# Kernel optimization log

Hardware: AMD Instinct MI355X
Metric: run time of the kernel (lower is better)

Reference implementation:

```python
import jax, jax.numpy as jnp
import numpy as np

B, NS, NT = 4, 512, 512
D_IN, C1, R, C2 = 128, 64, 32, 32
E = 32768
STEPS = 10


def setup_inputs() -> dict:
    key = jax.random.key(0)
    ks = jax.random.split(key, 12)
    inp = {}
    inp['x_s'] = jax.random.normal(ks[0], (B * NS, D_IN), jnp.float32)
    inp['edge_index_s'] = jax.random.randint(ks[1], (2, E), 0, B * NS, jnp.int32)
    inp['edge_attr_s'] = jax.random.uniform(ks[2], (E,), jnp.float32)
    inp['batch_s'] = (jnp.arange(B * NS, dtype=jnp.int32) // NS)
    inp['x_t'] = jax.random.normal(ks[3], (B * NT, D_IN), jnp.float32)
    inp['edge_index_t'] = jax.random.randint(ks[4], (2, E), 0, B * NT, jnp.int32)
    inp['edge_attr_t'] = jax.random.uniform(ks[5], (E,), jnp.float32)
    inp['batch_t'] = (jnp.arange(B * NT, dtype=jnp.int32) // NT)
    inp['W1'] = jax.random.normal(ks[6], (D_IN, C1), jnp.float32) / np.float32(np.sqrt(D_IN))
    inp['W2'] = jax.random.normal(ks[7], (R, C2), jnp.float32) / np.float32(np.sqrt(R))
    inp['mw1'] = jax.random.normal(ks[8], (C2, C2), jnp.float32) / np.float32(np.sqrt(C2))
    inp['mb1'] = jnp.zeros((C2,), jnp.float32)
    inp['mw2'] = jax.random.normal(ks[9], (C2, 1), jnp.float32) / np.float32(np.sqrt(C2))
    inp['mb2'] = jnp.zeros((1,), jnp.float32)
    inp['r'] = jax.random.normal(ks[10], (STEPS, B, NS, R), jnp.float32)
    return inp


def psi(x, src, dst, ea, W, n):
    # simple message-passing GNN: edge-weighted neighbor aggregation + linear + ReLU
    m = jax.ops.segment_sum(x[src] * ea[:, None], dst, num_segments=n)
    return jax.nn.relu((x + m) @ W)


def reference(x_s, edge_index_s, edge_attr_s, batch_s, x_t, edge_index_t, edge_attr_t,
              batch_t, W1, W2, mw1, mb1, mw2, mb2, r):
    # Uniform graph sizes -> to_dense_batch is a reshape and all masks are True,
    # so masked_softmax reduces to plain softmax; batch_s/batch_t kept for interface fidelity.
    ss, ds = edge_index_s[0], edge_index_s[1]
    st, dt = edge_index_t[0], edge_index_t[1]
    h_s = psi(x_s, ss, ds, edge_attr_s, W1, B * NS).reshape(B, NS, C1)
    h_t = psi(x_t, st, dt, edge_attr_t, W1, B * NT).reshape(B, NT, C1)
    S_hat0 = jnp.einsum('bsc,btc->bst', h_s, h_t)  # [B, NS, NT]
    S_0 = jax.nn.softmax(S_hat0, axis=-1)

    def step(S_hat, r_i):
        S = jax.nn.softmax(S_hat, axis=-1)
        r_t = jnp.einsum('bst,bsr->btr', S, r_i)  # S^T @ r_s
        o_s = psi(r_i.reshape(B * NS, R), ss, ds, edge_attr_s, W2, B * NS).reshape(B, NS, C2)
        o_t = psi(r_t.reshape(B * NT, R), st, dt, edge_attr_t, W2, B * NT).reshape(B, NT, C2)
        Dm = o_s[:, :, None, :] - o_t[:, None, :, :]  # [B, NS, NT, C2] outer difference
        upd = (jax.nn.relu(Dm @ mw1 + mb1) @ mw2 + mb2)[..., 0]
        return S_hat + upd, None

    S_hat, _ = jax.lax.scan(step, S_hat0, r)
    S_L = jax.nn.softmax(S_hat, axis=-1)
    return (S_0, S_L)
```

## Files before the change

kernel.cpp:

```cpp
#include <hip/hip_runtime.h>


constexpr int kB = 4;
constexpr int kNS = 512;
constexpr int kNT = 512;
constexpr int kDin = 128;
constexpr int kC1 = 64;
constexpr int kR = 32;
constexpr int kC2 = 32;
constexpr int kE = 32768;
constexpr int kSteps = 10;
constexpr int kN = kB * kNS;
constexpr int kEP = kE + 16 * kN;
constexpr int kChunkStride = kR * kN;

__global__ void k_hist(const int* __restrict__ ei_s, const int* __restrict__ ei_t,
                       int* __restrict__ deg) {
  int g = blockIdx.y;
  const int* dst = (g ? ei_t : ei_s) + kE;
  int e = blockIdx.x * 256 + threadIdx.x;
  atomicAdd(&deg[g * kN + dst[e]], 1);
}

__global__ void k_scan(const int* __restrict__ deg, int* __restrict__ off,
                       int* __restrict__ cur) {
  int g = blockIdx.x;
  const int* d = deg + g * kN;
  int* o = off + g * (kN + 1);
  int* c = cur + g * kN;
  __shared__ int sums[256];
  int tid = threadIdx.x;
  int loc[8];
  int s = 0;
#pragma unroll
  for (int i = 0; i < 8; ++i) {
    loc[i] = (d[tid * 8 + i] + 15) & ~15;
    s += loc[i];
  }
  sums[tid] = s;
  __syncthreads();
  for (int st = 1; st < 256; st <<= 1) {
    int v = (tid >= st) ? sums[tid - st] : 0;
    __syncthreads();
    sums[tid] += v;
    __syncthreads();
  }
  int base = (tid > 0) ? sums[tid - 1] : 0;
#pragma unroll
  for (int i = 0; i < 8; ++i) {
    int idx = tid * 8 + i;
    o[idx] = base;
    c[idx] = base;
    base += loc[i];
  }
  if (tid == 255) o[kN] = base;
}

__global__ void k_scatter(const int* __restrict__ ei_s, const int* __restrict__ ei_t,
                          const float* __restrict__ ea_s, const float* __restrict__ ea_t,
                          int* __restrict__ cur, int* __restrict__ srcs,
                          float* __restrict__ eaw) {
  int g = blockIdx.y;
  const int* ei = g ? ei_t : ei_s;
  const float* ea = g ? ea_t : ea_s;
  int e = blockIdx.x * 256 + threadIdx.x;
  int d = ei[kE + e];
  int srcv = ei[e];
  int pos = atomicAdd(&cur[g * kN + d], 1);
  srcs[g * kEP + pos] = srcv;
  eaw[g * kEP + pos] = ea[e];
}

__device__ __forceinline__ void psi2_node(
    int n, const float* __restrict__ vin, const int* __restrict__ sr,
    const float* __restrict__ ew, const int* __restrict__ o,
    const float* __restrict__ W2, const float* __restrict__ mw1,
    const float* __restrict__ mb1, const float* __restrict__ mw2w,
    float* __restrict__ Pout, float* __restrict__ ctOut) {
  int lane = threadIdx.x & 63;
  int f = lane & 31, hh = lane >> 5;
  int beg = o[n], end = o[n + 1];
  float m = 0.f;
  for (int b0 = beg + hh * 8; b0 < end; b0 += 16) {
#pragma unroll
    for (int q = 0; q < 8; ++q)
      m += vin[(size_t)sr[b0 + q] * kR + f] * ew[b0 + q];
  }
  m += __shfl_down(m, 32, 64);
  float v = vin[(size_t)n * kR + f] + m;
  float acc = 0.f;
#pragma unroll
  for (int k = 0; k < kC2; ++k) acc += __shfl(v, k, 64) * W2[k * kC2 + f];
  float ov = fmaxf(acc, 0.f);
  float p = mb1 ? mb1[f] : 0.f;
#pragma unroll
  for (int k = 0; k < kC2; ++k) p += __shfl(ov, k, 64) * mw1[k * kC2 + f];
  if (lane < 32) Pout[(size_t)n * kC2 + f] = p;
  if (ctOut) {
    float c = p * mw2w[f];
#pragma unroll
    for (int o2 = 16; o2; o2 >>= 1) c += __shfl_xor(c, o2, 64);
    if (lane == 0) ctOut[n] = c;
  }
}

__global__ __launch_bounds__(256) void k_pre(
    const float* __restrict__ x_s, const float* __restrict__ x_t,
    const float* __restrict__ r, const int* __restrict__ srcs,
    const float* __restrict__ eaw, const int* __restrict__ off,
    const float* __restrict__ W1, const float* __restrict__ W2,
    const float* __restrict__ mw1, const float* __restrict__ mb1,
    float* __restrict__ h, float* __restrict__ PsAll) {
  int bid = blockIdx.x, tid = threadIdx.x;
  if (bid < 2048) {
    int g = bid >> 10;
    int n = (bid & 1023) * 2 + (tid >> 7);
    int f = tid & 127;
    const float* x = g ? x_t : x_s;
    const int* sr = srcs + g * kEP;
    const float* ew = eaw + g * kEP;
    const int* o = off + g * (kN + 1);
    float* ho = h + (size_t)g * kN * kC1;
    __shared__ float y[2][kDin];
    int beg = o[n], end = o[n + 1];
    float xself = x[(size_t)n * kDin + f];
    float m = 0.f;
    for (int idx = beg; idx < end; idx += 8) {
      float a0 = x[(size_t)sr[idx + 0] * kDin + f] * ew[idx + 0];
      float a1 = x[(size_t)sr[idx + 1] * kDin + f] * ew[idx + 1];
      float a2 = x[(size_t)sr[idx + 2] * kDin + f] * ew[idx + 2];
      float a3 = x[(size_t)sr[idx + 3] * kDin + f] * ew[idx + 3];
      float a4 = x[(size_t)sr[idx + 4] * kDin + f] * ew[idx + 4];
      float a5 = x[(size_t)sr[idx + 5] * kDin + f] * ew[idx + 5];
      float a6 = x[(size_t)sr[idx + 6] * kDin + f] * ew[idx + 6];
      float a7 = x[(size_t)sr[idx + 7] * kDin + f] * ew[idx + 7];
      m += ((a0 + a1) + (a2 + a3)) + ((a4 + a5) + (a6 + a7));
    }
    y[tid >> 7][f] = xself + m;
    __syncthreads();
    if (f < kC1) {
      const float* yy = y[tid >> 7];
      float acc = 0.f;
#pragma unroll 16
      for (int k = 0; k < kDin; ++k) acc += yy[k] * W1[k * kC1 + f];
      ho[(size_t)n * kC1 + f] = fmaxf(acc, 0.f);
    }
  } else {
    int nn = (bid - 2048) * 4 + (tid >> 6);
    int step = nn >> 11, node = nn & (kN - 1);
    psi2_node(node, r + (size_t)step * kN * kR, srcs, eaw, off, W2, mw1, mb1,
              nullptr, PsAll + (size_t)step * kN * kR, nullptr);
  }
}

__global__ __launch_bounds__(256) void k_shat0(const float* __restrict__ h,
                                               float* __restrict__ Shat,
                                               float* __restrict__ pstatm,
                                               float* __restrict__ pstatl) {
  int b = blockIdx.z, s0 = blockIdx.y * 64, t0 = blockIdx.x * 64;
  const float* hs = h + (size_t)(b * kNS + s0) * kC1;
  const float* ht = h + (size_t)kN * kC1 + (size_t)(b * kNT + t0) * kC1;
  __shared__ float As[64 * 68];
  __shared__ float Bs[64 * 68];
  int tid = threadIdx.x;
#pragma unroll
  for (int k2 = 0; k2 < 4; ++k2) {
    int idx = tid + k2 * 256;
    int row = idx >> 4, c4 = idx & 15;
    float4 va = *(const float4*)(hs + (size_t)row * kC1 + c4 * 4);
    *(float4*)&As[row * 68 + c4 * 4] = va;
    float4 vb = *(const float4*)(ht + (size_t)row * kC1 + c4 * 4);
    *(float4*)&Bs[row * 68 + c4 * 4] = vb;
  }
  __syncthreads();
  int ts = tid >> 4, tt = tid & 15;
  float acc[4][4] = {};
#pragma unroll
  for (int cc = 0; cc < 16; ++cc) {
    float4 a[4], bt[4];
#pragma unroll
    for (int i = 0; i < 4; ++i) a[i] = *(const float4*)&As[(ts * 4 + i) * 68 + cc * 4];
#pragma unroll
    for (int k = 0; k < 4; ++k) bt[k] = *(const float4*)&Bs[(tt + 16 * k) * 68 + cc * 4];
#pragma unroll
    for (int i = 0; i < 4; ++i)
#pragma unroll
      for (int k = 0; k < 4; ++k)
        acc[i][k] += a[i].x * bt[k].x + a[i].y * bt[k].y + a[i].z * bt[k].z + a[i].w * bt[k].w;
  }
#pragma unroll
  for (int i = 0; i < 4; ++i) {
    int s = s0 + ts * 4 + i;
    float* row = Shat + (size_t)(b * kNS + s) * kNT;
#pragma unroll
    for (int k = 0; k < 4; ++k) row[t0 + tt + 16 * k] = acc[i][k];
  }
#pragma unroll
  for (int i = 0; i < 4; ++i) {
    float mm = fmaxf(fmaxf(acc[i][0], acc[i][1]), fmaxf(acc[i][2], acc[i][3]));
#pragma unroll
    for (int o2 = 8; o2; o2 >>= 1) mm = fmaxf(mm, __shfl_xor(mm, o2, 64));
    float se = 0.f;
#pragma unroll
    for (int k = 0; k < 4; ++k) se += __expf(acc[i][k] - mm);
#pragma unroll
    for (int o2 = 8; o2; o2 >>= 1) se += __shfl_xor(se, o2, 64);
    if (tt == 0) {
      int grow = b * kNS + s0 + ts * 4 + i;
      pstatm[blockIdx.x * kN + grow] = mm;
      pstatl[blockIdx.x * kN + grow] = se;
    }
  }
}

__global__ __launch_bounds__(256) void k_rt(const float* __restrict__ Shat,
                                            const float* __restrict__ pstatm,
                                            const float* __restrict__ pstatl,
                                            const float* __restrict__ ri,
                                            float* __restrict__ part, int nc,
                                            float* __restrict__ Sout) {
  int b = blockIdx.z, cs = blockIdx.y, s0 = cs * 64, t0 = blockIdx.x * 32;
  __shared__ float Wt[64 * 32];
  __shared__ float rch[64 * 32];
  __shared__ float lm[64], ll[64];
  int tid = threadIdx.x;
  if (tid < 64) {
    int row = b * kNS + s0 + tid;
    float m = -3.4e38f;
    for (int c = 0; c < nc; ++c) m = fmaxf(m, pstatm[c * kN + row]);
    float l = 0.f;
    for (int c = 0; c < nc; ++c) l += __expf(pstatm[c * kN + row] - m) * pstatl[c * kN + row];
    lm[tid] = m;
    ll[tid] = 1.f / l;
  }
  __syncthreads();
#pragma unroll
  for (int k2 = 0; k2 < 2; ++k2) {
    int idx = tid + k2 * 256;
    int row = idx >> 3, c4 = idx & 7;
    int grow = b * kNS + s0 + row;
    float4 v = *(const float4*)(Shat + (size_t)grow * kNT + t0 + c4 * 4);
    float m = lm[row], l = ll[row];
    float4 wv;
    wv.x = __expf(v.x - m) * l;
    wv.y = __expf(v.y - m) * l;
    wv.z = __expf(v.z - m) * l;
    wv.w = __expf(v.w - m) * l;
    *(float4*)&Wt[row * 32 + c4 * 4] = wv;
    if (Sout) *(float4*)(Sout + (size_t)grow * kNT + t0 + c4 * 4) = wv;
    float4 rv = *(const float4*)(ri + (size_t)grow * kR + c4 * 4);
    *(float4*)&rch[row * 32 + c4 * 4] = rv;
  }
  __syncthreads();
  int t_l = tid & 31, jg = tid >> 5;
  float4 acc = make_float4(0.f, 0.f, 0.f, 0.f);
  for (int s = 0; s < 64; ++s) {
    float wv = Wt[s * 32 + t_l];
    float4 rv = *(const float4*)&rch[s * 32 + jg * 4];
    acc.x += wv * rv.x; acc.y += wv * rv.y; acc.z += wv * rv.z; acc.w += wv * rv.w;
  }
  int gcol = b * kNT + t0 + t_l;
  float* dst = part + (size_t)cs * kChunkStride + (size_t)jg * 4 * kN + gcol;
  dst[0] = acc.x;
  dst[(size_t)kN] = acc.y;
  dst[(size_t)2 * kN] = acc.z;
  dst[(size_t)3 * kN] = acc.w;
}

__global__ __launch_bounds__(256) void k_red(const float* __restrict__ part,
                                             float* __restrict__ rt) {
  int idx = blockIdx.x * 256 + threadIdx.x;
  int j = idx >> 11, col = idx & (kN - 1);
  float s = 0.f;
#pragma unroll
  for (int cs = 0; cs < 8; ++cs) s += part[(size_t)cs * kChunkStride + idx];
  rt[(size_t)col * kR + j] = s;
}

__global__ __launch_bounds__(256) void k_psi2t(
    const float* __restrict__ rt, const int* __restrict__ srcs,
    const float* __restrict__ eaw, const int* __restrict__ off,
    const float* __restrict__ W2, const float* __restrict__ mw1,
    const float* __restrict__ mw2, float* __restrict__ Pt,
    float* __restrict__ ct) {
  int n = blockIdx.x * 4 + (threadIdx.x >> 6);
  psi2_node(n, rt, srcs + kEP, eaw + kEP, off + (kN + 1), W2, mw1, nullptr,
            mw2, Pt, ct);
}

__global__ __launch_bounds__(256) void k_upd(
    float* __restrict__ Shat, const float* __restrict__ Ps,
    const float* __restrict__ Pt, const float* __restrict__ ctb,
    const float* __restrict__ mw2, const float* __restrict__ mb2,
    float* __restrict__ pstatm, float* __restrict__ pstatl) {
  __shared__ float pts[256 * 33];
  __shared__ float red[8 * 4];
  __shared__ float lmx[8];
  int tid = threadIdx.x;
  int g0 = blockIdx.x * 8;
  int cc = blockIdx.y;
  int bb = g0 >> 9;
  int c0 = cc * 256;
  const float4* PtB = (const float4*)(Pt + ((size_t)bb * kNT + c0) * kC2);
#pragma unroll
  for (int k = 0; k < 8; ++k) {
    int idx = tid + k * 256;
    int col = idx >> 3, q = idx & 7;
    float4 v = PtB[idx];
    float* d = &pts[col * 33 + q * 4];
    d[0] = v.x; d[1] = v.y; d[2] = v.z; d[3] = v.w;
  }
  float old[8];
#pragma unroll
  for (int s = 0; s < 8; ++s) old[s] = Shat[(size_t)(g0 + s) * kNT + c0 + tid];
  float ctv = ctb[(size_t)bb * kNT + c0 + tid];
  __syncthreads();
  float pt[32];
#pragma unroll
  for (int j = 0; j < 32; ++j) pt[j] = pts[tid * 33 + j];
  float bias = mb2[0] - ctv;
  float nv[8];
#pragma unroll
  for (int s = 0; s < 8; ++s) {
    const float* psr = Ps + (size_t)(g0 + s) * kC2;
    float u = 0.f;
#pragma unroll
    for (int j = 0; j < 32; ++j) u += fmaxf(psr[j], pt[j]) * mw2[j];
    float v = old[s] + u + bias;
    Shat[(size_t)(g0 + s) * kNT + c0 + tid] = v;
    nv[s] = v;
  }
  int wv = tid >> 6, ln = tid & 63;
#pragma unroll
  for (int s = 0; s < 8; ++s) {
    float m = nv[s];
#pragma unroll
    for (int o2 = 32; o2; o2 >>= 1) m = fmaxf(m, __shfl_down(m, o2, 64));
    if (ln == 0) red[s * 4 + wv] = m;
  }
  __syncthreads();
  if (tid < 8) {
    lmx[tid] = fmaxf(fmaxf(red[tid * 4], red[tid * 4 + 1]),
                     fmaxf(red[tid * 4 + 2], red[tid * 4 + 3]));
  }
  __syncthreads();
#pragma unroll
  for (int s = 0; s < 8; ++s) {
    float e = __expf(nv[s] - lmx[s]);
#pragma unroll
    for (int o2 = 32; o2; o2 >>= 1) e += __shfl_down(e, o2, 64);
    if (ln == 0) red[s * 4 + wv] = e;
  }
  __syncthreads();
  if (tid < 8) {
    float l = red[tid * 4] + red[tid * 4 + 1] + red[tid * 4 + 2] + red[tid * 4 + 3];
    pstatm[cc * kN + g0 + tid] = lmx[tid];
    pstatl[cc * kN + g0 + tid] = l;
  }
}

__global__ __launch_bounds__(256) void k_out(const float* __restrict__ Shat,
                                             const float* __restrict__ pstatm,
                                             const float* __restrict__ pstatl,
                                             float* __restrict__ out) {
  int row = blockIdx.x, tid = threadIdx.x;
  float m0 = pstatm[row], m1 = pstatm[kN + row];
  float l0 = pstatl[row], l1 = pstatl[kN + row];
  float m = fmaxf(m0, m1);
  float linv = 1.f / (__expf(m0 - m) * l0 + __expf(m1 - m) * l1);
  const float* p = Shat + (size_t)row * kNT;
  float* d = out + (size_t)row * kNT;
  d[tid] = __expf(p[tid] - m) * linv;
  d[tid + 256] = __expf(p[tid + 256] - m) * linv;
}

extern "C" void kernel_launch(void* const* d_in, const int* in_sizes, int n_in,
                              void* d_out, int out_size, void* d_ws, size_t ws_size,
                              hipStream_t stream) {
  (void)in_sizes; (void)n_in; (void)out_size; (void)ws_size;
  const float* x_s = (const float*)d_in[0];
  const int* ei_s = (const int*)d_in[1];
  const float* ea_s = (const float*)d_in[2];
  const float* x_t = (const float*)d_in[4];
  const int* ei_t = (const int*)d_in[5];
  const float* ea_t = (const float*)d_in[6];
  const float* W1 = (const float*)d_in[8];
  const float* W2 = (const float*)d_in[9];
  const float* mw1 = (const float*)d_in[10];
  const float* mb1 = (const float*)d_in[11];
  const float* mw2 = (const float*)d_in[12];
  const float* mb2 = (const float*)d_in[13];
  const float* r = (const float*)d_in[14];
  float* out = (float*)d_out;

  char* w = (char*)d_ws;
  auto alloc = [&](size_t bytes) -> void* {
    void* p = (void*)w;
    w += (bytes + 255) & ~(size_t)255;
    return p;
  };
  int* deg = (int*)alloc((size_t)2 * kN * 4);
  int* cur = (int*)alloc((size_t)2 * kN * 4);
  int* srcs = (int*)alloc((size_t)2 * kEP * 4);
  float* eaw = (float*)alloc((size_t)2 * kEP * 4);
  size_t zbytes = (size_t)((char*)(eaw + 2 * kEP) - (char*)deg);
  int* off = (int*)alloc((size_t)2 * (kN + 1) * 4);
  float* h = (float*)alloc((size_t)2 * kN * kC1 * 4);
  float* Shat = (float*)alloc((size_t)kB * kNS * kNT * 4);
  float* pstatm = (float*)alloc((size_t)8 * kN * 4);
  float* pstatl = (float*)alloc((size_t)8 * kN * 4);
  float* rt = (float*)alloc((size_t)kN * kR * 4);
  float* PsAll = (float*)alloc((size_t)kSteps * kN * kR * 4);
  float* Pt = (float*)alloc((size_t)kN * kC2 * 4);
  float* ct = (float*)alloc((size_t)kN * 4);
  float* part = (float*)alloc((size_t)8 * kChunkStride * 4);

  hipMemsetAsync(deg, 0, zbytes, stream);
  k_hist<<<dim3(kE / 256, 2), 256, 0, stream>>>(ei_s, ei_t, deg);
  k_scan<<<2, 256, 0, stream>>>(deg, off, cur);
  k_scatter<<<dim3(kE / 256, 2), 256, 0, stream>>>(ei_s, ei_t, ea_s, ea_t, cur, srcs, eaw);
  k_pre<<<7168, 256, 0, stream>>>(x_s, x_t, r, srcs, eaw, off, W1, W2, mw1, mb1,
                                  h, PsAll);
  k_shat0<<<dim3(8, 8, kB), 256, 0, stream>>>(h, Shat, pstatm, pstatl);
  k_rt<<<dim3(16, 8, kB), 256, 0, stream>>>(Shat, pstatm, pstatl, r, part, 8, out);
  k_red<<<kChunkStride / 256, 256, 0, stream>>>(part, rt);
  for (int i = 0; i < kSteps; ++i) {
    k_psi2t<<<kN / 4, 256, 0, stream>>>(rt, srcs, eaw, off, W2, mw1, mw2, Pt, ct);
    k_upd<<<dim3(kN / 8, 2), 256, 0, stream>>>(Shat, PsAll + (size_t)i * kN * kR,
                                               Pt, ct, mw2, mb2, pstatm, pstatl);
    if (i + 1 < kSteps) {
      k_rt<<<dim3(16, 8, kB), 256, 0, stream>>>(Shat, pstatm, pstatl,
                                                r + (size_t)(i + 1) * kN * kR, part,
                                                2, nullptr);
      k_red<<<kChunkStride / 256, 256, 0, stream>>>(part, rt);
    }
  }
  k_out<<<kN, 256, 0, stream>>>(Shat, pstatm, pstatl, out + (size_t)kB * kNS * kNT);
}
```

Baseline: 428.4 us.

## Fuse S_hat update, softmax and S^T r partial products into one kernel

Adds k_updrt, which updates a full 512-wide row block of S_hat, computes the exact row softmax in-block and immediately accumulates the S^T·r_next partial products into 64 chunk buffers. This removes the separate k_rt pass that re-read S_hat every step and the two-chunk softmax statistics merge. k_red now sums 64 partial chunks instead of 8, and k_out takes a single-chunk path. The fused path runs only when the workspace is large enough, otherwise the old path is used. In exchange it writes and reduces more partial data per step and uses 512-thread blocks holding more registers.

After: 493.6 us. 15.2% more time.

```diff
diff --git a/kernel.cpp b/kernel.cpp
--- a/kernel.cpp
+++ b/kernel.cpp
@@ -268,12 +268,12 @@
 }
 
 __global__ __launch_bounds__(256) void k_red(const float* __restrict__ part,
-                                             float* __restrict__ rt) {
+                                             float* __restrict__ rt, int nc) {
   int idx = blockIdx.x * 256 + threadIdx.x;
   int j = idx >> 11, col = idx & (kN - 1);
   float s = 0.f;
-#pragma unroll
-  for (int cs = 0; cs < 8; ++cs) s += part[(size_t)cs * kChunkStride + idx];
+#pragma unroll 8
+  for (int cs = 0; cs < nc; ++cs) s += part[(size_t)cs * kChunkStride + idx];
   rt[(size_t)col * kR + j] = s;
 }
 
@@ -286,6 +286,105 @@
   int n = blockIdx.x * 4 + (threadIdx.x >> 6);
   psi2_node(n, rt, srcs + kEP, eaw + kEP, off + (kN + 1), W2, mw1, nullptr,
             mw2, Pt, ct);
+}
+
+__global__ __launch_bounds__(512) void k_updrt(
+    float* __restrict__ Shat, const float* __restrict__ Ps,
+    const float* __restrict__ Pt, const float* __restrict__ ctb,
+    const float* __restrict__ mw2, const float* __restrict__ mb2,
+    const float* __restrict__ rnext, float* __restrict__ part,
+    float* __restrict__ pstatm, float* __restrict__ pstatl) {
+  __shared__ float red[64];
+  __shared__ float lmx[8], llv[8];
+  __shared__ float r_lds[256];
+  int tid = threadIdx.x;
+  int g0 = blockIdx.x * 8;
+  int bb = g0 >> 9;
+  int gcol = bb * kNT + tid;
+  float pt[32];
+  {
+    const float4* pp = (const float4*)(Pt + (size_t)gcol * kC2);
+#pragma unroll
+    for (int q = 0; q < 8; ++q) {
+      float4 v = pp[q];
+      pt[q * 4 + 0] = v.x; pt[q * 4 + 1] = v.y;
+      pt[q * 4 + 2] = v.z; pt[q * 4 + 3] = v.w;
+    }
+  }
+  float ctv = ctb[gcol];
+  float old[8];
+#pragma unroll
+  for (int s = 0; s < 8; ++s) old[s] = Shat[(size_t)(g0 + s) * kNT + tid];
+  if (rnext && tid < 256) r_lds[tid] = rnext[(size_t)g0 * kR + tid];
+  float bias = mb2[0] - ctv;
+  float nv[8];
+#pragma unroll
+  for (int s = 0; s < 8; ++s) {
+    const float* psr = Ps + (size_t)(g0 + s) * kC2;
+    float u = 0.f;
+#pragma unroll
+    for (int j = 0; j < 32; ++j) u += fmaxf(psr[j], pt[j]) * mw2[j];
+    nv[s] = old[s] + u + bias;
+    Shat[(size_t)(g0 + s) * kNT + tid] = nv[s];
+  }
+  int wv = tid >> 6, ln = tid & 63;
+#pragma unroll
+  for (int s = 0; s < 8; ++s) {
+    float m = nv[s];
+#pragma unroll
+    for (int o2 = 32; o2; o2 >>= 1) m = fmaxf(m, __shfl_xor(m, o2, 64));
+    if (ln == 0) red[s * 8 + wv] = m;
+  }
+  __syncthreads();
+  if (tid < 8) {
+    float m = red[tid * 8];
+#pragma unroll
+    for (int w2 = 1; w2 < 8; ++w2) m = fmaxf(m, red[tid * 8 + w2]);
+    lmx[tid] = m;
+  }
+  __syncthreads();
+  float e[8];
+#pragma unroll
+  for (int s = 0; s < 8; ++s) {
+    e[s] = __expf(nv[s] - lmx[s]);
+    float t = e[s];
+#pragma unroll
+    for (int o2 = 32; o2; o2 >>= 1) t += __shfl_xor(t, o2, 64);
+    if (ln == 0) red[s * 8 + wv] = t;
+  }
+  __syncthreads();
+  if (tid < 8) {
+    float l = red[tid * 8] + red[tid * 8 + 1] + red[tid * 8 + 2] + red[tid * 8 + 3] +
+              red[tid * 8 + 4] + red[tid * 8 + 5] + red[tid * 8 + 6] + red[tid * 8 + 7];
+    llv[tid] = 1.f / l;
+    pstatm[g0 + tid] = lmx[tid];
+    pstatl[g0 + tid] = l;
+  }
+  __syncthreads();
+  if (!rnext) return;
+  float4 acc[8];
+#pragma unroll
+  for (int q = 0; q < 8; ++q) acc[q] = make_float4(0.f, 0.f, 0.f, 0.f);
+#pragma unroll
+  for (int s = 0; s < 8; ++s) {
+    float wgt = e[s] * llv[s];
+    const float4* rr = (const float4*)&r_lds[s * 32];
+#pragma unroll
+    for (int q = 0; q < 8; ++q) {
+      float4 rv = rr[q];
+      acc[q].x += wgt * rv.x; acc[q].y += wgt * rv.y;
+      acc[q].z += wgt * rv.z; acc[q].w += wgt * rv.w;
+    }
+  }
+  int grp = blockIdx.x & 63;
+  float* dst = part + (size_t)grp * kChunkStride + gcol;
+#pragma unroll
+  for (int q = 0; q < 8; ++q) {
+    dst[(size_t)(q * 4 + 0) * kN] = acc[q].x;
+    dst[(size_t)(q * 4 + 1) * kN] = acc[q].y;
+    dst[(size_t)(q * 4 + 2) * kN] = acc[q].z;
+    dst[(size_t)(q * 4 + 3) * kN] = acc[q].w;
+  }
 }
 
 __global__ __launch_bounds__(256) void k_upd(
@@ -362,12 +461,18 @@
 __global__ __launch_bounds__(256) void k_out(const float* __restrict__ Shat,
                                              const float* __restrict__ pstatm,
                                              const float* __restrict__ pstatl,
-                                             float* __restrict__ out) {
+                                             float* __restrict__ out, int nchunks) {
   int row = blockIdx.x, tid = threadIdx.x;
-  float m0 = pstatm[row], m1 = pstatm[kN + row];
-  float l0 = pstatl[row], l1 = pstatl[kN + row];
-  float m = fmaxf(m0, m1);
-  float linv = 1.f / (__expf(m0 - m) * l0 + __expf(m1 - m) * l1);
+  float m, linv;
+  if (nchunks == 2) {
+    float m0 = pstatm[row], m1 = pstatm[kN + row];
+    float l0 = pstatl[row], l1 = pstatl[kN + row];
+    m = fmaxf(m0, m1);
+    linv = 1.f / (__expf(m0 - m) * l0 + __expf(m1 - m) * l1);
+  } else {
+    m = pstatm[row];
+    linv = 1.f / pstatl[row];
+  }
   const float* p = Shat + (size_t)row * kNT;
   float* d = out + (size_t)row * kNT;
   d[tid] = __expf(p[tid] - m) * linv;
@@ -377,7 +482,7 @@
 extern "C" void kernel_launch(void* const* d_in, const int* in_sizes, int n_in,
                               void* d_out, int out_size, void* d_ws, size_t ws_size,
                               hipStream_t stream) {
-  (void)in_sizes; (void)n_in; (void)out_size; (void)ws_size;
+  (void)in_sizes; (void)n_in; (void)out_size;
   const float* x_s = (const float*)d_in[0];
   const int* ei_s = (const int*)d_in[1];
   const float* ea_s = (const float*)d_in[2];
@@ -413,7 +518,10 @@
   float* PsAll = (float*)alloc((size_t)kSteps * kN * kR * 4);
   float* Pt = (float*)alloc((size_t)kN * kC2 * 4);
   float* ct = (float*)alloc((size_t)kN * 4);
-  float* part = (float*)alloc((size_t)8 * kChunkStride * 4);
+  size_t base_used = (size_t)(w - (char*)d_ws);
+  bool big = (ws_size == 0) ||
+             (ws_size >= base_used + (size_t)64 * kChunkStride * 4 + 4096);
+  float* part = (float*)alloc((size_t)(big ? 64 : 8) * kChunkStride * 4);
 
   hipMemsetAsync(deg, 0, zbytes, stream);
   k_hist<<<dim3(kE / 256, 2), 256, 0, stream>>>(ei_s, ei_t, deg);
@@ -423,17 +531,31 @@
                                   h, PsAll);
   k_shat0<<<dim3(8, 8, kB), 256, 0, stream>>>(h, Shat, pstatm, pstatl);
   k_rt<<<dim3(16, 8, kB), 256, 0, stream>>>(Shat, pstatm, pstatl, r, part, 8, out);
-  k_red<<<kChunkStride / 256, 256, 0, stream>>>(part, rt);
-  for (int i = 0; i < kSteps; ++i) {
-    k_psi2t<<<kN / 4, 256, 0, stream>>>(rt, srcs, eaw, off, W2, mw1, mw2, Pt, ct);
-    k_upd<<<dim3(kN / 8, 2), 256, 0, stream>>>(Shat, PsAll + (size_t)i * kN * kR,
-                                               Pt, ct, mw2, mb2, pstatm, pstatl);
-    if (i + 1 < kSteps) {
-      k_rt<<<dim3(16, 8, kB), 256, 0, stream>>>(Shat, pstatm, pstatl,
-                                                r + (size_t)(i + 1) * kN * kR, part,
-                                                2, nullptr);
-      k_red<<<kChunkStride / 256, 256, 0, stream>>>(part, rt);
-    }
-  }
-  k_out<<<kN, 256, 0, stream>>>(Shat, pstatm, pstatl, out + (size_t)kB * kNS * kNT);
-}
+  k_red<<<kChunkStride / 256, 256, 0, stream>>>(part, rt, 8);
+  if (big) {
+    for (int i = 0; i < kSteps; ++i) {
+      k_psi2t<<<kN / 4, 256, 0, stream>>>(rt, srcs, eaw, off, W2, mw1, mw2, Pt, ct);
+      const float* rnext = (i + 1 < kSteps) ? r + (size_t)(i + 1) * kN * kR : nullptr;
+      k_updrt<<<kN / 8, 512, 0, stream>>>(Shat, PsAll + (size_t)i * kN * kR, Pt,
+                                          ct, mw2, mb2, rnext, part, pstatm, pstatl);
+      if (i + 1 < kSteps)
+        k_red<<<kChunkStride / 256, 256, 0, stream>>>(part, rt, 64);
+    }
+    k_out<<<kN, 256, 0, stream>>>(Shat, pstatm, pstatl,
+                                  out + (size_t)kB * kNS * kNT, 1);
+  } else {
+    for (int i = 0; i < kSteps; ++i) {
+      k_psi2t<<<kN / 4, 256, 0, stream>>>(rt, srcs, eaw, off, W2, mw1, mw2, Pt, ct);
+      k_upd<<<dim3(kN / 8, 2), 256, 0, stream>>>(Shat, PsAll + (size_t)i * kN * kR,
+                                                 Pt, ct, mw2, mb2, pstatm, pstatl);
+      if (i + 1 < kSteps) {
+        k_rt<<<dim3(16, 8, kB), 256, 0, stream>>>(Shat, pstatm, pstatl,
+                                                  r + (size_t)(i + 1) * kN * kR, part,
+                                                  2, nullptr);
+        k_red<<<kChunkStride / 256, 256, 0, stream>>>(part, rt, 8);
+      }
+    }
+    k_out<<<kN, 256, 0, stream>>>(Shat, pstatm, pstatl,
+                                  out + (size_t)kB * kNS * kNT, 2);
+  }
+}
```
